# Kernel tuning notes

Measured on AMD Instinct MI355X. Metric: run time of the kernel, lower is better.

Reference implementation:

```python
import jax, jax.numpy as jnp
from jax import lax
import numpy as np

D_MODEL = 1024
D_STATE = 16
D_CONV = 4
EXPAND = 2
D_INNER = EXPAND * D_MODEL
BATCH = 2
SEQLEN = 1024


def setup_inputs() -> dict:
    key = jax.random.key(0)
    ks = jax.random.split(key, 8)
    x = jax.random.normal(ks[0], (BATCH, SEQLEN, D_MODEL), jnp.float32)
    W_in = jax.random.normal(ks[1], (2 * D_INNER, D_MODEL), jnp.float32) * (1.0 / np.sqrt(D_MODEL))
    conv_w = jax.random.normal(ks[2], (D_INNER, 1, D_CONV), jnp.float32) * (1.0 / np.sqrt(D_CONV))
    conv_b = jax.random.normal(ks[3], (D_INNER,), jnp.float32) * 0.02
    W_x = jax.random.normal(ks[4], (2 * D_STATE, D_INNER), jnp.float32) * (1.0 / np.sqrt(D_INNER))
    W_dt = jax.random.normal(ks[5], (D_INNER, D_INNER), jnp.float32) * (1.0 / np.sqrt(D_INNER))
    b_dt = jax.random.normal(ks[6], (D_INNER,), jnp.float32) * 0.02
    # A_log = log(arange(1..d_state)) repeated over d_inner rows, as in __init__
    A_log = jnp.log(jnp.tile(jnp.arange(1, D_STATE + 1, dtype=jnp.float32), (D_INNER, 1)))
    D = jnp.ones((D_INNER,), jnp.float32)
    W_out = jax.random.normal(ks[7], (D_MODEL, D_INNER), jnp.float32) * (1.0 / np.sqrt(D_INNER))
    return {"x": x, "W_in": W_in, "conv_w": conv_w, "conv_b": conv_b,
            "W_x": W_x, "W_dt": W_dt, "b_dt": b_dt, "A_log": A_log,
            "D": D, "W_out": W_out}


def reference(x, W_in, conv_w, conv_b, W_x, W_dt, b_dt, A_log, D, W_out):
    d_inner, _, d_conv = conv_w.shape
    d_state = A_log.shape[1]

    # in_proj and split into x / gate z
    xz = x @ W_in.T                                   # (B, L, 2*d_inner)
    xi, z = jnp.split(xz, 2, axis=-1)

    # causal depthwise conv1d: torch pads both sides by d_conv-1 then slices
    # [:seqlen], which equals left-only padding of d_conv-1
    xc = lax.conv_general_dilated(
        xi.transpose(0, 2, 1), conv_w, window_strides=(1,),
        padding=[(d_conv - 1, 0)],
        dimension_numbers=("NCH", "OIH", "NCH"),
        feature_group_count=d_inner)
    xc = xc + conv_b[None, :, None]
    u = jax.nn.silu(xc.transpose(0, 2, 1))            # (B, L, d_inner)

    # input-dependent B, C and dt
    BC = u @ W_x.T                                    # (B, L, 2*d_state)
    Bmat, Cmat = jnp.split(BC, 2, axis=-1)
    dt = jax.nn.softplus(u @ W_dt.T + b_dt)           # (B, L, d_inner)

    A = -jnp.exp(A_log)                               # (d_inner, d_state)
    dA = jnp.exp(dt[..., None] * A)                   # (B, L, d_inner, d_state)
    dBu = dt[..., None] * Bmat[:, :, None, :] * u[..., None]

    def step(s, inp):
        dA_t, dBu_t, C_t = inp
        s = dA_t * s + dBu_t                          # (B, d_inner, d_state)
        y_t = jnp.einsum("bdn,bn->bd", s, C_t)
        return s, y_t

    s0 = jnp.zeros((x.shape[0], d_inner, d_state), x.dtype)
    _, ys = lax.scan(step, s0,
                     (dA.transpose(1, 0, 2, 3),
                      dBu.transpose(1, 0, 2, 3),
                      Cmat.transpose(1, 0, 2)))
    y = ys.transpose(1, 0, 2) + D * u                 # (B, L, d_inner)

    y = y * jax.nn.silu(z)
    # dropout is identity in eval mode
    return y @ W_out.T
```

## Files before the change

kernel.cpp:

```cpp
#include <hip/hip_runtime.h>
#include <hip/hip_bf16.h>
#include <math.h>

#define B_SZ   2
#define LSEQ   1024
#define DMODEL 1024
#define DSTATE 16
#define DCONV  4
#define DINNER 2048
#define MROWS  (B_SZ * LSEQ)
#define NCHUNK 32
#define TCHUNK (LSEQ / NCHUNK)
#define NCAT   2176

typedef __attribute__((ext_vector_type(8))) short bf16x8;
typedef __attribute__((ext_vector_type(4))) float f32x4;

__device__ __forceinline__ void gl2lds16(const void* g, void* l) {
    __builtin_amdgcn_global_load_lds(
        (const __attribute__((address_space(1))) void*)g,
        (__attribute__((address_space(3))) void*)l, 16, 0, 0);
}

__global__ __launch_bounds__(256)
void cvt_bf16(const float* __restrict__ in, __hip_bfloat16* __restrict__ out)
{
    int i = (blockIdx.x * 256 + threadIdx.x) * 8;
    float4 a = *(const float4*)&in[i];
    float4 b = *(const float4*)&in[i + 4];
    union { __hip_bfloat16 h[8]; int4 v; } o;
    o.h[0] = __float2bfloat16(a.x); o.h[1] = __float2bfloat16(a.y);
    o.h[2] = __float2bfloat16(a.z); o.h[3] = __float2bfloat16(a.w);
    o.h[4] = __float2bfloat16(b.x); o.h[5] = __float2bfloat16(b.y);
    o.h[6] = __float2bfloat16(b.z); o.h[7] = __float2bfloat16(b.w);
    *(int4*)&out[i] = o.v;
}

template<int EPI, int BN>
__global__ __launch_bounds__(256)
void gemm_bt(const __hip_bfloat16* __restrict__ A,
             const __hip_bfloat16* __restrict__ B,
             const float* __restrict__ bias,
             float* __restrict__ C0, float* __restrict__ C1,
             int ldc, float* __restrict__ C2,
             int K, int klen)
{
    constexpr int NFR  = BN / 32;
    constexpr int NCH  = (128 + BN) / 16;
    constexpr int NLD  = NCH / 4;
    constexpr int SMEL = (128 + BN) * 32;
    __shared__ __hip_bfloat16 sm[2 * SMEL];

    const int tid  = threadIdx.x;
    const int lane = tid & 63;
    const int w    = tid >> 6;
    const int m0 = blockIdx.x * 128;
    const int n0 = blockIdx.y * BN;
    const int wr = w >> 1, wc = w & 1;
    const int kbase = blockIdx.z * klen;
    float* __restrict__ C = (blockIdx.z == 0) ? C0 : C1;

    const int lrow = lane >> 2;
    const int scol = (lane & 3) * 8;
    const __hip_bfloat16* srcp[NLD];
    #pragma unroll
    for (int i = 0; i < NLD; ++i) {
        const int q = w + 4 * i;
        srcp[i] = (q < 8)
            ? A + (size_t)(m0 + q * 16 + lrow) * K + scol + kbase
            : B + (size_t)(n0 + (q - 8) * 16 + lrow) * K + scol + kbase;
    }

    f32x4 acc[4][NFR] = {};

    #pragma unroll
    for (int i = 0; i < NLD; ++i)
        gl2lds16(srcp[i], sm + (w + 4 * i) * 512);
    __syncthreads();

    const int nt = klen / 32;
    int cur = 0;
    for (int t = 0; t < nt; ++t) {
        if (t + 1 < nt) {
            const int nxt = cur ^ 1;
            #pragma unroll
            for (int i = 0; i < NLD; ++i)
                gl2lds16(srcp[i] + (size_t)(t + 1) * 32,
                         sm + nxt * SMEL + (w + 4 * i) * 512);
        }
        const __hip_bfloat16* As = sm + cur * SMEL;
        const __hip_bfloat16* Bs = As + 128 * 32;
        bf16x8 af[4], bfr[NFR];
        const int ar = (wr * 64 + (lane & 15)) * 32 + (lane >> 4) * 8;
        const int br = (wc * (BN / 2) + (lane & 15)) * 32 + (lane >> 4) * 8;
        #pragma unroll
        for (int m = 0; m < 4; ++m)
            af[m] = *(const bf16x8*)&As[ar + m * 16 * 32];
        #pragma unroll
        for (int n = 0; n < NFR; ++n)
            bfr[n] = *(const bf16x8*)&Bs[br + n * 16 * 32];
        #pragma unroll
        for (int m = 0; m < 4; ++m)
            #pragma unroll
            for (int n = 0; n < NFR; ++n)
                acc[m][n] = __builtin_amdgcn_mfma_f32_16x16x32_bf16(
                    af[m], bfr[n], acc[m][n], 0, 0, 0);
        __syncthreads();
        cur ^= 1;
    }

    #pragma unroll
    for (int m = 0; m < 4; ++m) {
        #pragma unroll
        for (int n = 0; n < NFR; ++n) {
            const int col = n0 + wc * (BN / 2) + n * 16 + (lane & 15);
            #pragma unroll
            for (int j = 0; j < 4; ++j) {
                const int row = m0 + wr * 64 + m * 16 + (lane >> 4) * 4 + j;
                float v = acc[m][n][j];
                if (EPI == 0) {
                    C[(size_t)row * ldc + col] = v;
                } else {
                    if (col < DINNER) {
                        v += bias[col];
                        v = (v > 20.f) ? v : log1pf(__expf(v));
                        C0[(size_t)row * ldc + col] = v;
                    } else if (col < DINNER + 32) {
                        C2[(size_t)row * 32 + (col - DINNER)] = v;
                    }
                }
            }
        }
    }
}

__global__ __launch_bounds__(256)
void add2(const float* __restrict__ a, const float* __restrict__ b,
          float* __restrict__ o)
{
    int i = (blockIdx.x * 256 + threadIdx.x) * 4;
    float4 va = *(const float4*)&a[i];
    float4 vb = *(const float4*)&b[i];
    va.x += vb.x; va.y += vb.y; va.z += vb.z; va.w += vb.w;
    *(float4*)&o[i] = va;
}

__global__ __launch_bounds__(256)
void conv_silu(const float* __restrict__ xz, const float* __restrict__ cw,
               const float* __restrict__ cb, float* __restrict__ u,
               __hip_bfloat16* __restrict__ u_bf)
{
    int idx = blockIdx.x * blockDim.x + threadIdx.x;
    int d = idx & (DINNER - 1);
    int m = idx >> 11;
    int t = m & (LSEQ - 1);
    float acc = cb[d];
    #pragma unroll
    for (int j = 0; j < DCONV; ++j) {
        int tt = t - (DCONV - 1) + j;
        if (tt >= 0)
            acc += xz[(size_t)(m - t + tt) * 4096 + d] * cw[d * DCONV + j];
    }
    float v = acc / (1.f + __expf(-acc));
    u[(size_t)m * DINNER + d] = v;
    u_bf[(size_t)m * DINNER + d] = __float2bfloat16(v);
}

__global__ __launch_bounds__(256)
void scan_part1(const float* __restrict__ dt, const float* __restrict__ u,
                const float* __restrict__ bc, const float* __restrict__ A_log,
                float* __restrict__ s_end, float* __restrict__ dtsum)
{
    const int d = blockIdx.x * 256 + threadIdx.x;
    const int c = blockIdx.y;
    const int b = blockIdx.z;
    __shared__ float bcs[TCHUNK][32];
    {
        int f = threadIdx.x * 4;
        const float* src = bc + ((size_t)b * LSEQ + c * TCHUNK) * 32;
        *(float4*)&bcs[f >> 5][f & 31] = *(const float4*)&src[f];
    }
    float An[16];
    {
        float4 a0 = *(const float4*)&A_log[d * DSTATE + 0];
        float4 a1 = *(const float4*)&A_log[d * DSTATE + 4];
        float4 a2 = *(const float4*)&A_log[d * DSTATE + 8];
        float4 a3 = *(const float4*)&A_log[d * DSTATE + 12];
        An[0]=-__expf(a0.x); An[1]=-__expf(a0.y); An[2]=-__expf(a0.z); An[3]=-__expf(a0.w);
        An[4]=-__expf(a1.x); An[5]=-__expf(a1.y); An[6]=-__expf(a1.z); An[7]=-__expf(a1.w);
        An[8]=-__expf(a2.x); An[9]=-__expf(a2.y); An[10]=-__expf(a2.z); An[11]=-__expf(a2.w);
        An[12]=-__expf(a3.x); An[13]=-__expf(a3.y); An[14]=-__expf(a3.z); An[15]=-__expf(a3.w);
    }
    __syncthreads();
    const float* dtp = dt + ((size_t)b * LSEQ + c * TCHUNK) * DINNER + d;
    const float* up  = u  + ((size_t)b * LSEQ + c * TCHUNK) * DINNER + d;
    float s[16] = {};
    float sum = 0.f;
    for (int t = 0; t < TCHUNK; ++t) {
        float dtv = dtp[(size_t)t * DINNER];
        float uv  = up [(size_t)t * DINNER];
        sum += dtv;
        float du = dtv * uv;
        #pragma unroll
        for (int n = 0; n < 16; ++n) {
            float a = __expf(dtv * An[n]);
            s[n] = a * s[n] + du * bcs[t][n];
        }
    }
    float* se = s_end + ((size_t)(b * NCHUNK + c) * DINNER + d) * 16;
    #pragma unroll
    for (int q = 0; q < 4; ++q)
        *(float4*)&se[q * 4] = make_float4(s[q*4], s[q*4+1], s[q*4+2], s[q*4+3]);
    dtsum[(size_t)(b * NCHUNK + c) * DINNER + d] = sum;
}

__global__ __launch_bounds__(256)
void scan_combine(float* __restrict__ s_end, const float* __restrict__ dtsum,
                  const float* __restrict__ A_log)
{
    int idx = blockIdx.x * 256 + threadIdx.x;
    int n = idx & 15;
    int d = (idx >> 4) & (DINNER - 1);
    int b = idx >> 15;
    float An = -__expf(A_log[d * DSTATE + n]);
    float s = 0.f;
    for (int c = 0; c < NCHUNK; ++c) {
        size_t base = (size_t)(b * NCHUNK + c) * DINNER + d;
        float se = s_end[base * 16 + n];
        s_end[base * 16 + n] = s;
        float P = __expf(An * dtsum[base]);
        s = P * s + se;
    }
}

__global__ __launch_bounds__(256)
void scan_part2(const float* __restrict__ dt, const float* __restrict__ u,
                const float* __restrict__ bc, const float* __restrict__ s_in,
                const float* __restrict__ A_log, const float* __restrict__ Dp,
                const float* __restrict__ xz, __hip_bfloat16* __restrict__ y_bf)
{
    const int d = blockIdx.x * 256 + threadIdx.x;
    const int c = blockIdx.y;
    const int b = blockIdx.z;
    __shared__ float bcs[TCHUNK][32];
    {
        int f = threadIdx.x * 4;
        const float* src = bc + ((size_t)b * LSEQ + c * TCHUNK) * 32;
        *(float4*)&bcs[f >> 5][f & 31] = *(const float4*)&src[f];
    }
    float An[16];
    {
        float4 a0 = *(const float4*)&A_log[d * DSTATE + 0];
        float4 a1 = *(const float4*)&A_log[d * DSTATE + 4];
        float4 a2 = *(const float4*)&A_log[d * DSTATE + 8];
        float4 a3 = *(const float4*)&A_log[d * DSTATE + 12];
        An[0]=-__expf(a0.x); An[1]=-__expf(a0.y); An[2]=-__expf(a0.z); An[3]=-__expf(a0.w);
        An[4]=-__expf(a1.x); An[5]=-__expf(a1.y); An[6]=-__expf(a1.z); An[7]=-__expf(a1.w);
        An[8]=-__expf(a2.x); An[9]=-__expf(a2.y); An[10]=-__expf(a2.z); An[11]=-__expf(a2.w);
        An[12]=-__expf(a3.x); An[13]=-__expf(a3.y); An[14]=-__expf(a3.z); An[15]=-__expf(a3.w);
    }
    float s[16];
    {
        const float* si = s_in + ((size_t)(b * NCHUNK + c) * DINNER + d) * 16;
        #pragma unroll
        for (int q = 0; q < 4; ++q) {
            float4 v = *(const float4*)&si[q * 4];
            s[q*4] = v.x; s[q*4+1] = v.y; s[q*4+2] = v.z; s[q*4+3] = v.w;
        }
    }
    const float Dd = Dp[d];
    __syncthreads();
    const float* dtp = dt + ((size_t)b * LSEQ + c * TCHUNK) * DINNER + d;
    const float* up  = u  + ((size_t)b * LSEQ + c * TCHUNK) * DINNER + d;
    const float* zp  = xz + ((size_t)b * LSEQ + c * TCHUNK) * 4096 + 2048 + d;
    __hip_bfloat16* yp = y_bf + ((size_t)b * LSEQ + c * TCHUNK) * DINNER + d;
    for (int t = 0; t < TCHUNK; ++t) {
        float dtv = dtp[(size_t)t * DINNER];
        float uv  = up [(size_t)t * DINNER];
        float du = dtv * uv;
        float y = Dd * uv;
        #pragma unroll
        for (int n = 0; n < 16; ++n) {
            float a = __expf(dtv * An[n]);
            s[n] = a * s[n] + du * bcs[t][n];
            y += s[n] * bcs[t][16 + n];
        }
        float zv = zp[(size_t)t * 4096];
        yp[(size_t)t * DINNER] = __float2bfloat16(y * (zv / (1.f + __expf(-zv))));
    }
}

extern "C" void kernel_launch(void* const* d_in, const int* in_sizes, int n_in,
                              void* d_out, int out_size, void* d_ws, size_t ws_size,
                              hipStream_t stream)
{
    const float* x      = (const float*)d_in[0];
    const float* W_in   = (const float*)d_in[1];
    const float* conv_w = (const float*)d_in[2];
    const float* conv_b = (const float*)d_in[3];
    const float* W_x    = (const float*)d_in[4];
    const float* W_dt   = (const float*)d_in[5];
    const float* b_dt   = (const float*)d_in[6];
    const float* A_log  = (const float*)d_in[7];
    const float* Dp     = (const float*)d_in[8];
    const float* W_out  = (const float*)d_in[9];
    float* out = (float*)d_out;

    const size_t MB = 1ull << 20;
    char* w8 = (char*)d_ws;
    float* xz    = (float*)(w8);
    float* u     = (float*)(w8 + 32*MB);
    float* dt    = (float*)(w8 + 48*MB);
    float* bc    = (float*)(w8 + 64*MB);
    float* sbuf  = (float*)(w8 + 65*MB);
    float* dtsum = (float*)(w8 + 73*MB);
    __hip_bfloat16* u_bf   = (__hip_bfloat16*)(w8 + 74*MB);
    __hip_bfloat16* x_bf   = (__hip_bfloat16*)(w8 + 82*MB);
    __hip_bfloat16* Win_bf = (__hip_bfloat16*)(w8 + 86*MB);
    __hip_bfloat16* Wcat_bf= (__hip_bfloat16*)(w8 + 82*MB);
    __hip_bfloat16* Wout_bf= (__hip_bfloat16*)(w8 + 91*MB);
    __hip_bfloat16* y_bf   = (__hip_bfloat16*)(w8 + 82*MB);
    float* p0 = (float*)(w8);
    float* p1 = (float*)(w8 + 8*MB);

    cvt_bf16<<<(MROWS * DMODEL) / (256 * 8), 256, 0, stream>>>(x, x_bf);
    cvt_bf16<<<(4096 * DMODEL) / (256 * 8), 256, 0, stream>>>(W_in, Win_bf);
    gemm_bt<0, 128><<<dim3(16, 32, 1), 256, 0, stream>>>(
        x_bf, Win_bf, nullptr, xz, xz, 4096, nullptr, DMODEL, DMODEL);
    conv_silu<<<(MROWS * DINNER) / 256, 256, 0, stream>>>(xz, conv_w, conv_b, u, u_bf);
    cvt_bf16<<<(DINNER * DINNER) / (256 * 8), 256, 0, stream>>>(W_dt, Wcat_bf);
    cvt_bf16<<<(32 * DINNER) / (256 * 8), 256, 0, stream>>>(W_x, Wcat_bf + (size_t)DINNER * DINNER);
    cvt_bf16<<<(DMODEL * DINNER) / (256 * 8), 256, 0, stream>>>(W_out, Wout_bf);
    gemm_bt<2, 64><<<dim3(16, NCAT / 64, 1), 256, 0, stream>>>(
        u_bf, Wcat_bf, b_dt, dt, dt, DINNER, bc, DINNER, DINNER);
    scan_part1<<<dim3(DINNER/256, NCHUNK, B_SZ), 256, 0, stream>>>(
        dt, u, bc, A_log, sbuf, dtsum);
    scan_combine<<<(B_SZ * DINNER * DSTATE) / 256, 256, 0, stream>>>(
        sbuf, dtsum, A_log);
    scan_part2<<<dim3(DINNER/256, NCHUNK, B_SZ), 256, 0, stream>>>(
        dt, u, bc, sbuf, A_log, Dp, xz, y_bf);
    gemm_bt<0, 64><<<dim3(16, 16, 2), 256, 0, stream>>>(
        y_bf, Wout_bf, nullptr, p0, p1, DMODEL, nullptr, DINNER, DINNER / 2);
    add2<<<(MROWS * DMODEL) / (256 * 4), 256, 0, stream>>>(p0, p1, out);
}
```

Measured before the change: 197.2 us.

## Triple-buffer GEMM LDS pipeline with one barrier per step; 2-wave BN=64 tiles

```diff
diff --git a/kernel.cpp b/kernel.cpp
--- a/kernel.cpp
+++ b/kernel.cpp
@@ -37,7 +37,7 @@
 }
 
 template<int EPI, int BN>
-__global__ __launch_bounds__(256)
+__global__ __launch_bounds__((BN == 128) ? 256 : 128)
 void gemm_bt(const __hip_bfloat16* __restrict__ A,
              const __hip_bfloat16* __restrict__ B,
              const float* __restrict__ bias,
@@ -45,18 +45,19 @@
              int ldc, float* __restrict__ C2,
              int K, int klen)
 {
-    constexpr int NFR  = BN / 32;
-    constexpr int NCH  = (128 + BN) / 16;
-    constexpr int NLD  = NCH / 4;
-    constexpr int SMEL = (128 + BN) * 32;
-    __shared__ __hip_bfloat16 sm[2 * SMEL];
+    constexpr int WAVES = (BN == 128) ? 4 : 2;
+    constexpr int NCH   = (128 + BN) / 16;
+    constexpr int NLD   = NCH / WAVES;
+    constexpr int SMEL  = (128 + BN) * 32;
+    __shared__ __hip_bfloat16 sm[3 * SMEL];
 
     const int tid  = threadIdx.x;
     const int lane = tid & 63;
     const int w    = tid >> 6;
     const int m0 = blockIdx.x * 128;
     const int n0 = blockIdx.y * BN;
-    const int wr = w >> 1, wc = w & 1;
+    const int wr = (BN == 128) ? (w >> 1) : w;
+    const int wc = (BN == 128) ? (w & 1)  : 0;
     const int kbase = blockIdx.z * klen;
     float* __restrict__ C = (blockIdx.z == 0) ? C0 : C1;
 
@@ -65,55 +66,71 @@
     const __hip_bfloat16* srcp[NLD];
     #pragma unroll
     for (int i = 0; i < NLD; ++i) {
-        const int q = w + 4 * i;
+        const int q = w + WAVES * i;
         srcp[i] = (q < 8)
             ? A + (size_t)(m0 + q * 16 + lrow) * K + scol + kbase
             : B + (size_t)(n0 + (q - 8) * 16 + lrow) * K + scol + kbase;
     }
 
-    f32x4 acc[4][NFR] = {};
+    f32x4 acc[4][4] = {};
 
     #pragma unroll
     for (int i = 0; i < NLD; ++i)
-        gl2lds16(srcp[i], sm + (w + 4 * i) * 512);
-    __syncthreads();
+        gl2lds16(srcp[i], sm + (w + WAVES * i) * 512);
+    #pragma unroll
+    for (int i = 0; i < NLD; ++i)
+        gl2lds16(srcp[i] + 32, sm + SMEL + (w + WAVES * i) * 512);
 
     const int nt = klen / 32;
-    int cur = 0;
-    for (int t = 0; t < nt; ++t) {
-        if (t + 1 < nt) {
-            const int nxt = cur ^ 1;
+    const int ar = (wr * 64 + (lane & 15)) * 32 + (lane >> 4) * 8;
+    const int br = (wc * 64 + (lane & 15)) * 32 + (lane >> 4) * 8;
+
+    auto compute = [&](int bufi) {
+        const __hip_bfloat16* As = sm + bufi * SMEL;
+        const __hip_bfloat16* Bs = As + 128 * 32;
+        bf16x8 af[4], bfr[4];
+        #pragma unroll
+        for (int m = 0; m < 4; ++m)
+            af[m] = *(const bf16x8*)&As[ar + m * 16 * 32];
+        #pragma unroll
+        for (int n = 0; n < 4; ++n)
+            bfr[n] = *(const bf16x8*)&Bs[br + n * 16 * 32];
+        #pragma unroll
+        for (int m = 0; m < 4; ++m)
+            #pragma unroll
+            for (int n = 0; n < 4; ++n)
+                acc[m][n] = __builtin_amdgcn_mfma_f32_16x16x32_bf16(
+                    af[m], bfr[n], acc[m][n], 0, 0, 0);
+    };
+
+    int cb = 0;
+    for (int t = 0; t < nt - 1; ++t) {
+        if constexpr (NLD == 4)
+            asm volatile("s_waitcnt vmcnt(4)" ::: "memory");
+        else
+            asm volatile("s_waitcnt vmcnt(6)" ::: "memory");
+        __builtin_amdgcn_s_barrier();
+        __builtin_amdgcn_sched_barrier(0);
+        if (t + 2 < nt) {
+            int db = cb + 2; if (db >= 3) db -= 3;
             #pragma unroll
             for (int i = 0; i < NLD; ++i)
-                gl2lds16(srcp[i] + (size_t)(t + 1) * 32,
-                         sm + nxt * SMEL + (w + 4 * i) * 512);
-        }
-        const __hip_bfloat16* As = sm + cur * SMEL;
-        const __hip_bfloat16* Bs = As + 128 * 32;
-        bf16x8 af[4], bfr[NFR];
-        const int ar = (wr * 64 + (lane & 15)) * 32 + (lane >> 4) * 8;
-        const int br = (wc * (BN / 2) + (lane & 15)) * 32 + (lane >> 4) * 8;
-        #pragma unroll
-        for (int m = 0; m < 4; ++m)
-            af[m] = *(const bf16x8*)&As[ar + m * 16 * 32];
-        #pragma unroll
-        for (int n = 0; n < NFR; ++n)
-            bfr[n] = *(const bf16x8*)&Bs[br + n * 16 * 32];
-        #pragma unroll
-        for (int m = 0; m < 4; ++m)
-            #pragma unroll
-            for (int n = 0; n < NFR; ++n)
-                acc[m][n] = __builtin_amdgcn_mfma_f32_16x16x32_bf16(
-                    af[m], bfr[n], acc[m][n], 0, 0, 0);
-        __syncthreads();
-        cur ^= 1;
-    }
+                gl2lds16(srcp[i] + (size_t)(t + 2) * 32,
+                         sm + db * SMEL + (w + WAVES * i) * 512);
+        }
+        compute(cb);
+        cb = (cb == 2) ? 0 : cb + 1;
+    }
+    asm volatile("s_waitcnt vmcnt(0)" ::: "memory");
+    __builtin_amdgcn_s_barrier();
+    __builtin_amdgcn_sched_barrier(0);
+    compute(cb);
 
     #pragma unroll
     for (int m = 0; m < 4; ++m) {
         #pragma unroll
-        for (int n = 0; n < NFR; ++n) {
-            const int col = n0 + wc * (BN / 2) + n * 16 + (lane & 15);
+        for (int n = 0; n < 4; ++n) {
+            const int col = n0 + wc * 64 + n * 16 + (lane & 15);
             #pragma unroll
             for (int j = 0; j < 4; ++j) {
                 const int row = m0 + wr * 64 + m * 16 + (lane >> 4) * 4 + j;
@@ -331,7 +348,7 @@
     cvt_bf16<<<(DINNER * DINNER) / (256 * 8), 256, 0, stream>>>(W_dt, Wcat_bf);
     cvt_bf16<<<(32 * DINNER) / (256 * 8), 256, 0, stream>>>(W_x, Wcat_bf + (size_t)DINNER * DINNER);
     cvt_bf16<<<(DMODEL * DINNER) / (256 * 8), 256, 0, stream>>>(W_out, Wout_bf);
-    gemm_bt<2, 64><<<dim3(16, NCAT / 64, 1), 256, 0, stream>>>(
+    gemm_bt<2, 64><<<dim3(16, NCAT / 64, 1), 128, 0, stream>>>(
         u_bf, Wcat_bf, b_dt, dt, dt, DINNER, bc, DINNER, DINNER);
     scan_part1<<<dim3(DINNER/256, NCHUNK, B_SZ), 256, 0, stream>>>(
         dt, u, bc, A_log, sbuf, dtsum);
@@ -339,7 +356,7 @@
         sbuf, dtsum, A_log);
     scan_part2<<<dim3(DINNER/256, NCHUNK, B_SZ), 256, 0, stream>>>(
         dt, u, bc, sbuf, A_log, Dp, xz, y_bf);
-    gemm_bt<0, 64><<<dim3(16, 16, 2), 256, 0, stream>>>(
+    gemm_bt<0, 64><<<dim3(16, 16, 2), 128, 0, stream>>>(
         y_bf, Wout_bf, nullptr, p0, p1, DMODEL, nullptr, DINNER, DINNER / 2);
     add2<<<(MROWS * DMODEL) / (256 * 4), 256, 0, stream>>>(p0, p1, out);
 }
```

After: 212.6 us. 7.8% more time.

## Use BK=64 swizzled LDS tiles in GEMM and split output projection K four ways

Applied to the files above, without the earlier changes.

```diff
diff --git a/kernel.cpp b/kernel.cpp
--- a/kernel.cpp
+++ b/kernel.cpp
@@ -12,6 +12,7 @@
 #define NCHUNK 32
 #define TCHUNK (LSEQ / NCHUNK)
 #define NCAT   2176
+#define BKS    64
 
 typedef __attribute__((ext_vector_type(8))) short bf16x8;
 typedef __attribute__((ext_vector_type(4))) float f32x4;
@@ -36,19 +37,18 @@
     *(int4*)&out[i] = o.v;
 }
 
-template<int EPI, int BN>
+template<int EPI>
 __global__ __launch_bounds__(256)
 void gemm_bt(const __hip_bfloat16* __restrict__ A,
              const __hip_bfloat16* __restrict__ B,
              const float* __restrict__ bias,
-             float* __restrict__ C0, float* __restrict__ C1,
-             int ldc, float* __restrict__ C2,
+             float* __restrict__ Cbase, size_t pstride, int ldc,
+             float* __restrict__ C2,
              int K, int klen)
 {
-    constexpr int NFR  = BN / 32;
-    constexpr int NCH  = (128 + BN) / 16;
-    constexpr int NLD  = NCH / 4;
-    constexpr int SMEL = (128 + BN) * 32;
+    constexpr int BN   = 64;
+    constexpr int NLD  = (128 + BN) / 8 / 4;
+    constexpr int SMEL = (128 + BN) * BKS;
     __shared__ __hip_bfloat16 sm[2 * SMEL];
 
     const int tid  = threadIdx.x;
@@ -58,65 +58,78 @@
     const int n0 = blockIdx.y * BN;
     const int wr = w >> 1, wc = w & 1;
     const int kbase = blockIdx.z * klen;
-    float* __restrict__ C = (blockIdx.z == 0) ? C0 : C1;
-
-    const int lrow = lane >> 2;
-    const int scol = (lane & 3) * 8;
+    float* __restrict__ C = Cbase + (size_t)blockIdx.z * pstride;
+
+    const int lrow = lane >> 3;
+    const int swc  = ((lane & 7) ^ lrow) * 8;
     const __hip_bfloat16* srcp[NLD];
     #pragma unroll
     for (int i = 0; i < NLD; ++i) {
         const int q = w + 4 * i;
-        srcp[i] = (q < 8)
-            ? A + (size_t)(m0 + q * 16 + lrow) * K + scol + kbase
-            : B + (size_t)(n0 + (q - 8) * 16 + lrow) * K + scol + kbase;
-    }
-
-    f32x4 acc[4][NFR] = {};
+        srcp[i] = (q < 16)
+            ? A + (size_t)(m0 + q * 8 + lrow) * K + kbase + swc
+            : B + (size_t)(n0 + (q - 16) * 8 + lrow) * K + kbase + swc;
+    }
+
+    f32x4 acc[4][2] = {};
+    const int l7 = lane & 7, l15 = lane & 15, lq = lane >> 4;
+    const int sw0 = (lq ^ l7) * 8;
+    const int sw1 = sw0 ^ 32;
 
     #pragma unroll
     for (int i = 0; i < NLD; ++i)
         gl2lds16(srcp[i], sm + (w + 4 * i) * 512);
-    __syncthreads();
-
-    const int nt = klen / 32;
-    int cur = 0;
+    asm volatile("s_waitcnt vmcnt(0)" ::: "memory");
+    __builtin_amdgcn_s_barrier();
+    __builtin_amdgcn_sched_barrier(0);
+
+    const int nt = klen / BKS;
+    int buf = 0;
     for (int t = 0; t < nt; ++t) {
         if (t + 1 < nt) {
-            const int nxt = cur ^ 1;
             #pragma unroll
             for (int i = 0; i < NLD; ++i)
-                gl2lds16(srcp[i] + (size_t)(t + 1) * 32,
-                         sm + nxt * SMEL + (w + 4 * i) * 512);
-        }
-        const __hip_bfloat16* As = sm + cur * SMEL;
-        const __hip_bfloat16* Bs = As + 128 * 32;
-        bf16x8 af[4], bfr[NFR];
-        const int ar = (wr * 64 + (lane & 15)) * 32 + (lane >> 4) * 8;
-        const int br = (wc * (BN / 2) + (lane & 15)) * 32 + (lane >> 4) * 8;
-        #pragma unroll
-        for (int m = 0; m < 4; ++m)
-            af[m] = *(const bf16x8*)&As[ar + m * 16 * 32];
-        #pragma unroll
-        for (int n = 0; n < NFR; ++n)
-            bfr[n] = *(const bf16x8*)&Bs[br + n * 16 * 32];
+                gl2lds16(srcp[i] + (size_t)(t + 1) * BKS,
+                         sm + (buf ^ 1) * SMEL + (w + 4 * i) * 512);
+        }
+        const __hip_bfloat16* As = sm + buf * SMEL;
+        const __hip_bfloat16* Bs = As + 128 * BKS;
+        bf16x8 a0[4], a1[4], b0[2], b1[2];
+        #pragma unroll
+        for (int m = 0; m < 4; ++m) {
+            const int r = (wr * 64 + m * 16 + l15) * BKS;
+            a0[m] = *(const bf16x8*)&As[r + sw0];
+            a1[m] = *(const bf16x8*)&As[r + sw1];
+        }
+        #pragma unroll
+        for (int n = 0; n < 2; ++n) {
+            const int r = (wc * 32 + n * 16 + l15) * BKS;
+            b0[n] = *(const bf16x8*)&Bs[r + sw0];
+            b1[n] = *(const bf16x8*)&Bs[r + sw1];
+        }
         #pragma unroll
         for (int m = 0; m < 4; ++m)
             #pragma unroll
-            for (int n = 0; n < NFR; ++n)
+            for (int n = 0; n < 2; ++n) {
                 acc[m][n] = __builtin_amdgcn_mfma_f32_16x16x32_bf16(
-                    af[m], bfr[n], acc[m][n], 0, 0, 0);
-        __syncthreads();
-        cur ^= 1;
-    }
-
-    #pragma unroll
-    for (int m = 0; m < 4; ++m) {
-        #pragma unroll
-        for (int n = 0; n < NFR; ++n) {
-            const int col = n0 + wc * (BN / 2) + n * 16 + (lane & 15);
+                    a0[m], b0[n], acc[m][n], 0, 0, 0);
+                acc[m][n] = __builtin_amdgcn_mfma_f32_16x16x32_bf16(
+                    a1[m], b1[n], acc[m][n], 0, 0, 0);
+            }
+        asm volatile("s_waitcnt vmcnt(0)" ::: "memory");
+        __builtin_amdgcn_s_barrier();
+        __builtin_amdgcn_sched_barrier(0);
+        buf ^= 1;
+    }
+
+    #pragma unroll
+    for (int m = 0; m < 4; ++m)
+        #pragma unroll
+        for (int n = 0; n < 2; ++n) {
+            const int col = n0 + wc * 32 + n * 16 + l15;
             #pragma unroll
             for (int j = 0; j < 4; ++j) {
-                const int row = m0 + wr * 64 + m * 16 + (lane >> 4) * 4 + j;
+                const int row = m0 + wr * 64 + m * 16 + lq * 4 + j;
                 float v = acc[m][n][j];
                 if (EPI == 0) {
                     C[(size_t)row * ldc + col] = v;
@@ -124,25 +137,27 @@
                     if (col < DINNER) {
                         v += bias[col];
                         v = (v > 20.f) ? v : log1pf(__expf(v));
-                        C0[(size_t)row * ldc + col] = v;
+                        C[(size_t)row * ldc + col] = v;
                     } else if (col < DINNER + 32) {
                         C2[(size_t)row * 32 + (col - DINNER)] = v;
                     }
                 }
             }
         }
-    }
-}
-
-__global__ __launch_bounds__(256)
-void add2(const float* __restrict__ a, const float* __restrict__ b,
-          float* __restrict__ o)
-{
+}
+
+__global__ __launch_bounds__(256)
+void add4(const float* __restrict__ p, float* __restrict__ o)
+{
+    const size_t S = (size_t)MROWS * DMODEL;
     int i = (blockIdx.x * 256 + threadIdx.x) * 4;
-    float4 va = *(const float4*)&a[i];
-    float4 vb = *(const float4*)&b[i];
-    va.x += vb.x; va.y += vb.y; va.z += vb.z; va.w += vb.w;
-    *(float4*)&o[i] = va;
+    float4 a = *(const float4*)&p[i];
+    float4 b = *(const float4*)&p[i + S];
+    float4 c = *(const float4*)&p[i + 2 * S];
+    float4 d = *(const float4*)&p[i + 3 * S];
+    a.x += b.x + c.x + d.x; a.y += b.y + c.y + d.y;
+    a.z += b.z + c.z + d.z; a.w += b.w + c.w + d.w;
+    *(float4*)&o[i] = a;
 }
 
 __global__ __launch_bounds__(256)
@@ -309,8 +324,9 @@
     const size_t MB = 1ull << 20;
     char* w8 = (char*)d_ws;
     float* xz    = (float*)(w8);
+    float* p3    = (float*)(w8);
     float* u     = (float*)(w8 + 32*MB);
-    float* dt    = (float*)(w8 + 48*MB);
+    float* dtc   = (float*)(w8 + 48*MB);
     float* bc    = (float*)(w8 + 64*MB);
     float* sbuf  = (float*)(w8 + 65*MB);
     float* dtsum = (float*)(w8 + 73*MB);
@@ -318,28 +334,28 @@
     __hip_bfloat16* x_bf   = (__hip_bfloat16*)(w8 + 82*MB);
     __hip_bfloat16* Win_bf = (__hip_bfloat16*)(w8 + 86*MB);
     __hip_bfloat16* Wcat_bf= (__hip_bfloat16*)(w8 + 82*MB);
-    __hip_bfloat16* Wout_bf= (__hip_bfloat16*)(w8 + 91*MB);
+    __hip_bfloat16* Wout_bf= (__hip_bfloat16*)(w8 + 90*MB + 512*1024);
     __hip_bfloat16* y_bf   = (__hip_bfloat16*)(w8 + 82*MB);
-    float* p0 = (float*)(w8);
-    float* p1 = (float*)(w8 + 8*MB);
-
-    cvt_bf16<<<(MROWS * DMODEL) / (256 * 8), 256, 0, stream>>>(x, x_bf);
-    cvt_bf16<<<(4096 * DMODEL) / (256 * 8), 256, 0, stream>>>(W_in, Win_bf);
-    gemm_bt<0, 128><<<dim3(16, 32, 1), 256, 0, stream>>>(
-        x_bf, Win_bf, nullptr, xz, xz, 4096, nullptr, DMODEL, DMODEL);
+    Wout_bf = (__hip_bfloat16*)(w8 + 90*MB);
+
+    cvt_bf16<<<(MROWS * DMODEL) / 2048, 256, 0, stream>>>(x, x_bf);
+    cvt_bf16<<<(4096 * DMODEL) / 2048, 256, 0, stream>>>(W_in, Win_bf);
+    gemm_bt<0><<<dim3(16, 64, 1), 256, 0, stream>>>(
+        x_bf, Win_bf, nullptr, xz, 0, 4096, nullptr, DMODEL, DMODEL);
     conv_silu<<<(MROWS * DINNER) / 256, 256, 0, stream>>>(xz, conv_w, conv_b, u, u_bf);
-    cvt_bf16<<<(DINNER * DINNER) / (256 * 8), 256, 0, stream>>>(W_dt, Wcat_bf);
-    cvt_bf16<<<(32 * DINNER) / (256 * 8), 256, 0, stream>>>(W_x, Wcat_bf + (size_t)DINNER * DINNER);
-    cvt_bf16<<<(DMODEL * DINNER) / (256 * 8), 256, 0, stream>>>(W_out, Wout_bf);
-    gemm_bt<2, 64><<<dim3(16, NCAT / 64, 1), 256, 0, stream>>>(
-        u_bf, Wcat_bf, b_dt, dt, dt, DINNER, bc, DINNER, DINNER);
+    cvt_bf16<<<(DINNER * DINNER) / 2048, 256, 0, stream>>>(W_dt, Wcat_bf);
+    cvt_bf16<<<(32 * DINNER) / 2048, 256, 0, stream>>>(W_x, Wcat_bf + (size_t)DINNER * DINNER);
+    gemm_bt<2><<<dim3(16, NCAT / 64, 1), 256, 0, stream>>>(
+        u_bf, Wcat_bf, b_dt, dtc, 0, DINNER, bc, DINNER, DINNER);
+    cvt_bf16<<<(DMODEL * DINNER) / 2048, 256, 0, stream>>>(W_out, Wout_bf);
     scan_part1<<<dim3(DINNER/256, NCHUNK, B_SZ), 256, 0, stream>>>(
-        dt, u, bc, A_log, sbuf, dtsum);
+        dtc, u, bc, A_log, sbuf, dtsum);
     scan_combine<<<(B_SZ * DINNER * DSTATE) / 256, 256, 0, stream>>>(
         sbuf, dtsum, A_log);
     scan_part2<<<dim3(DINNER/256, NCHUNK, B_SZ), 256, 0, stream>>>(
-        dt, u, bc, sbuf, A_log, Dp, xz, y_bf);
-    gemm_bt<0, 64><<<dim3(16, 16, 2), 256, 0, stream>>>(
-        y_bf, Wout_bf, nullptr, p0, p1, DMODEL, nullptr, DINNER, DINNER / 2);
-    add2<<<(MROWS * DMODEL) / (256 * 4), 256, 0, stream>>>(p0, p1, out);
-}
+        dtc, u, bc, sbuf, A_log, Dp, xz, y_bf);
+    gemm_bt<0><<<dim3(16, 16, 4), 256, 0, stream>>>(
+        y_bf, Wout_bf, nullptr, p3, (size_t)MROWS * DMODEL, DMODEL, nullptr,
+        DINNER, DINNER / 4);
+    add4<<<(MROWS * DMODEL) / 1024, 256, 0, stream>>>(p3, out);
+}
```

New measurement: 194.4 us. Within noise of the previous version (-1.4%).
